# Kernel tuning notes

Measured on AMD Instinct MI355X. Metric: run time of the kernel, lower is better.

The kernel has to match this reference:

```python
import jax, jax.numpy as jnp
import numpy as np

BATCH, INPUTDIM, OUTDIM, GRIDSIZE = 4096, 256, 256, 64


def setup_inputs() -> dict:
    key = jax.random.key(0)
    k1, k2 = jax.random.split(key)
    x = jax.random.normal(k1, (BATCH, INPUTDIM), dtype=jnp.float32)
    # xavier_uniform over (2, outdim, inputdim, gridsize): fan_in = inputdim*gridsize, fan_out = outdim*gridsize
    fan_in = INPUTDIM * GRIDSIZE
    fan_out = OUTDIM * GRIDSIZE
    limit = float(np.sqrt(6.0 / (fan_in + fan_out)))
    fouriercoeffs = jax.random.uniform(
        k2, (2, OUTDIM, INPUTDIM, GRIDSIZE), dtype=jnp.float32,
        minval=-limit, maxval=limit)
    bias = jnp.zeros((1, OUTDIM), dtype=jnp.float32)
    return {"x": x, "fouriercoeffs": fouriercoeffs, "bias": bias}


def reference(x, fouriercoeffs, bias):
    # x: [B, inputdim]; fouriercoeffs: [2, outdim, inputdim, gridsize]; bias: [1, outdim]
    # gridsize_param is clamp/round'ed to an int in torch -> static = initial_gridsize here.
    G = fouriercoeffs.shape[-1]
    k = jnp.arange(1, G + 1, dtype=x.dtype)        # [G] frequencies 1..G
    xk = x[:, :, None] * k                          # [B, inputdim, G]
    c = jnp.cos(xk)                                 # [B, inputdim, G]
    s = jnp.sin(xk)                                 # [B, inputdim, G]
    # Fused contraction over (inputdim, gridsize) -- avoids the naive
    # [B, outdim, inputdim, gridsize] broadcast tensor of the torch code.
    y = (jnp.einsum('big,oig->bo', c, fouriercoeffs[0])
         + jnp.einsum('big,oig->bo', s, fouriercoeffs[1])
         + bias)                                    # [B, outdim]
    return y
```

## Files before the change

### kernel.cpp

```cpp
#include <hip/hip_runtime.h>
#include <hip/hip_bf16.h>


typedef __attribute__((ext_vector_type(8))) short short8;
typedef __attribute__((ext_vector_type(16))) float f32x16;

#define SPLITK 16
#define ICHUNK (256 / SPLITK)

#define INV2PI 0.15915494309189535f

__device__ __forceinline__ unsigned short f2bf(float f) {
    unsigned u = __builtin_bit_cast(unsigned, f);
    u += 0x7fffu + ((u >> 16) & 1u);
    return (unsigned short)(u >> 16);
}
#if __has_builtin(__builtin_amdgcn_cvt_pk_bf16_f32)
typedef __attribute__((ext_vector_type(2))) __bf16 bf16x2_t;
__device__ __forceinline__ unsigned pkbf16(float a, float b) {
    bf16x2_t v = __builtin_amdgcn_cvt_pk_bf16_f32(a, b);
    return __builtin_bit_cast(unsigned, v);
}
#else
__device__ __forceinline__ unsigned pkbf16(float a, float b) {
    unsigned ua = __builtin_bit_cast(unsigned, a) + 0x8000u;
    unsigned ub = __builtin_bit_cast(unsigned, b) + 0x8000u;
    return __builtin_amdgcn_perm(ub, ua, 0x07060302u);
}
#endif

__device__ __forceinline__ void dbl2(float c, float s, float& co, float& so) {
    float t = c + c;
    co = __builtin_fmaf(t, c, -1.f);
    so = t * s;
}
__device__ __forceinline__ void rot2(float c, float s, float cr, float sr,
                                     float& co, float& so) {
    float t = s * sr;
    co = __builtin_fmaf(c, cr, -t);
    float u = s * cr;
    so = __builtin_fmaf(c, sr, u);
}

__device__ __forceinline__ short8 chain8(float m1, float fm1, float f0) {
    unsigned r[4];
    float vp = fm1, v = f0;
    #pragma unroll
    for (int h = 0; h < 4; ++h) {
        float v1 = __builtin_fmaf(m1, v, -vp);
        r[h] = pkbf16(v, v1);
        float v2 = __builtin_fmaf(m1, v1, -v);
        vp = v1; v = v2;
    }
    uint4 u; u.x = r[0]; u.y = r[1]; u.z = r[2]; u.w = r[3];
    return __builtin_bit_cast(short8, u);
}

__device__ __forceinline__ void async_load16(const void* g, void* l) {
    __builtin_amdgcn_global_load_lds(
        (const __attribute__((address_space(1))) unsigned int*)g,
        (__attribute__((address_space(3))) unsigned int*)l,
        16, 0, 0);
}

__global__ __launch_bounds__(512) void prep_kernel(
    const float* __restrict__ fc, unsigned short* __restrict__ ws2)
{
    __shared__ unsigned pk[512][36];
    const int i = blockIdx.x;
    const int t = threadIdx.x;
    const int rr  = t >> 4;
    const int l16 = t & 15;

    #pragma unroll
    for (int p = 0; p < 16; ++p) {
        int r = p * 32 + rr;
        const float4* src =
            (const float4*)(fc + ((size_t)r * 256 + i) * 64) + l16;
        float4 v = *src;
        pk[r][l16 * 2]     = pkbf16(v.x, v.y);
        pk[r][l16 * 2 + 1] = pkbf16(v.z, v.w);
    }
    __syncthreads();

    #pragma unroll
    for (int gg = 0; gg < 8; ++gg) {
        int gi = gg * 512 + t;
        int sog = gi >> 6, ll = gi & 63;
        int ks = sog >> 3, cb = sog & 7;
        int o  = cb * 32 + (ll & 31);
        int kb = ks * 16 + (ll >> 5) * 8;
        int tt = kb >> 6, g0 = kb & 63;
        int r = tt * 256 + o;
        int c = g0 >> 1;
        uint4 v;
        v.x = pk[r][c]; v.y = pk[r][c + 1];
        v.z = pk[r][c + 2]; v.w = pk[r][c + 3];
        ((uint4*)ws2)[(size_t)i * 4096 + gi] = v;
    }
}

__global__ __launch_bounds__(256) void bias_init(
    const float* __restrict__ bias, float* __restrict__ out)
{
    int idx4 = blockIdx.x * 256 + threadIdx.x;
    ((float4*)out)[idx4] = ((const float4*)bias)[idx4 & 63];
}

__global__ __launch_bounds__(256) void reduce_kernel(
    const unsigned short* __restrict__ pws, const float* __restrict__ bias,
    float* __restrict__ out)
{
    int idx4 = blockIdx.x * 256 + threadIdx.x;
    float4 r = ((const float4*)bias)[idx4 & 63];
    #pragma unroll
    for (int z = 0; z < SPLITK; ++z) {
        ushort4 v = ((const ushort4*)pws)[(size_t)z * 262144 + idx4];
        r.x += __builtin_bit_cast(float, (unsigned)v.x << 16);
        r.y += __builtin_bit_cast(float, (unsigned)v.y << 16);
        r.z += __builtin_bit_cast(float, (unsigned)v.z << 16);
        r.w += __builtin_bit_cast(float, (unsigned)v.w << 16);
    }
    ((float4*)out)[idx4] = r;
}

template <bool USE_WS, bool PARTIAL>
__global__ __launch_bounds__(512, 2) void fkan_gemm(
    const float* __restrict__ x, const float* __restrict__ fc,
    const unsigned short* __restrict__ bws, float* __restrict__ out,
    unsigned short* __restrict__ pws)
{
    __shared__ uint4 Bflat[8192];
    __shared__ float xs[ICHUNK][256];

    const int t  = threadIdx.x;
    const int l  = t & 63;
    const int w  = t >> 6;
    const int rg = w >> 1;
    const int cg = w & 1;
    const int m32 = l & 31;
    const int h  = l >> 5;

    const int bid = blockIdx.x;
    const int z   = bid & 15;
    const int bx  = bid >> 4;
    const int rowBase = bx * 256;
    const int iBase   = z * ICHUNK;

    f32x16 acc[2][4];
    #pragma unroll
    for (int a = 0; a < 2; ++a)
        #pragma unroll
        for (int b = 0; b < 4; ++b) acc[a][b] = (f32x16)0.0f;

    short8 aF[2][8];

    auto stageHalf = [&](int slot, int j) {
        const uint4* base = (const uint4*)bws +
            (size_t)(iBase + (j >> 1)) * 4096 + (j & 1) * 2048;
        uint4* dst = Bflat + slot * 2048;
        #pragma unroll
        for (int cc = 0; cc < 4; ++cc) {
            int c = cc * 8 + w;
            async_load16(base + (size_t)c * 64 + l, (void*)(dst + c * 64));
        }
    };

    auto synth = [&](int ii) {
        #pragma unroll
        for (int rf = 0; rf < 2; ++rf) {
            float xv = xs[ii][rg * 64 + rf * 32 + m32];
            float rev = xv * INV2PI;
            float s1 = __builtin_amdgcn_sinf(rev);
            float c1 = __builtin_amdgcn_cosf(rev);
            const float m1 = c1 + c1;
            float c2, s2, c4, s4, c8, s8, c16, s16;
            dbl2(c1, s1, c2, s2);
            dbl2(c2, s2, c4, s4);
            dbl2(c4, s4, c8, s8);
            dbl2(c8, s8, c16, s16);
            float cB = h ? c8 : 1.f;
            float sB = h ? s8 : 0.f;
            #pragma unroll
            for (int k = 0; k < 4; ++k) {
                float cB1, sB1;
                rot2(cB, sB, c1, s1, cB1, sB1);
                aF[rf][k]     = chain8(m1, cB, cB1);
                aF[rf][4 + k] = chain8(m1, sB, sB1);
                if (k < 3) {
                    float cN, sN;
                    rot2(cB, sB, c16, s16, cN, sN);
                    cB = cN; sB = sN;
                }
            }
        }
    };

    auto mfmaHalf = [&](int slot,
                        short8 a00, short8 a01, short8 a02, short8 a03,
                        short8 a10, short8 a11, short8 a12, short8 a13) {
        const uint4* Bp = Bflat + slot * 2048;
        short8 a0v[4] = {a00, a01, a02, a03};
        short8 a1v[4] = {a10, a11, a12, a13};
        #pragma unroll
        for (int ks = 0; ks < 4; ++ks) {
            short8 bF[4];
            #pragma unroll
            for (int cf = 0; cf < 4; ++cf)
                bF[cf] = __builtin_bit_cast(short8,
                    Bp[(ks * 8 + cg * 4 + cf) * 64 + l]);
            #pragma unroll
            for (int cf = 0; cf < 4; ++cf) {
                acc[0][cf] = __builtin_amdgcn_mfma_f32_32x32x16_bf16(
                    a0v[ks], bF[cf], acc[0][cf], 0, 0, 0);
                acc[1][cf] = __builtin_amdgcn_mfma_f32_32x32x16_bf16(
                    a1v[ks], bF[cf], acc[1][cf], 0, 0, 0);
            }
        }
    };

    auto loadXs = [&]() {
        const int row = t >> 1;
        const int hf  = t & 1;
        const float4* px =
            (const float4*)(x + (size_t)(rowBase + row) * 256 + iBase) + hf * 2;
        float4 v0 = px[0], v1 = px[1];
        int c0 = hf * 8;
        xs[c0 + 0][row] = v0.x; xs[c0 + 1][row] = v0.y;
        xs[c0 + 2][row] = v0.z; xs[c0 + 3][row] = v0.w;
        xs[c0 + 4][row] = v1.x; xs[c0 + 5][row] = v1.y;
        xs[c0 + 6][row] = v1.z; xs[c0 + 7][row] = v1.w;
    };

    if constexpr (USE_WS) {
        loadXs();
        stageHalf(0, 0);
        stageHalf(1, 1);
        stageHalf(2, 2);
        asm volatile("s_waitcnt vmcnt(8) lgkmcnt(0)" ::: "memory");
        __builtin_amdgcn_s_barrier();
        asm volatile("" ::: "memory");

        #pragma unroll 1
        for (int jj = 0; jj < 16; ++jj) {
            const int j0 = jj * 2;

            if (jj <= 14) stageHalf((j0 + 3) & 3, j0 + 3);
            synth(jj);
            __builtin_amdgcn_s_setprio(1);
            mfmaHalf(j0 & 3,
                     aF[0][0], aF[0][1], aF[0][2], aF[0][3],
                     aF[1][0], aF[1][1], aF[1][2], aF[1][3]);
            __builtin_amdgcn_s_setprio(0);
            if (jj < 15) asm volatile("s_waitcnt vmcnt(8)" ::: "memory");
            else         asm volatile("s_waitcnt vmcnt(0)" ::: "memory");
            __builtin_amdgcn_s_barrier();
            asm volatile("" ::: "memory");

            if (jj <= 13) stageHalf((j0 + 4) & 3, j0 + 4);
            __builtin_amdgcn_s_setprio(1);
            mfmaHalf((j0 + 1) & 3,
                     aF[0][4], aF[0][5], aF[0][6], aF[0][7],
                     aF[1][4], aF[1][5], aF[1][6], aF[1][7]);
            __builtin_amdgcn_s_setprio(0);
            if (jj < 14) {
                asm volatile("s_waitcnt vmcnt(8)" ::: "memory");
                __builtin_amdgcn_s_barrier();
                asm volatile("" ::: "memory");
            } else if (jj == 14) {
                asm volatile("s_waitcnt vmcnt(4)" ::: "memory");
                __builtin_amdgcn_s_barrier();
                asm volatile("" ::: "memory");
            }
        }
    } else {
        auto stageBfc = [&](int p, int i) {
            #pragma unroll
            for (int gg = 0; gg < 8; ++gg) {
                int gi  = gg * 512 + t;
                int sog = gi >> 6, ll = gi & 63;
                int ks = sog >> 3, cb = sog & 7;
                int o  = cb * 32 + (ll & 31);
                int kb = ks * 16 + (ll >> 5) * 8;
                int tt = kb >> 6, g0 = kb & 63;
                const float4* p4 = (const float4*)(fc +
                    ((((size_t)tt * 256 + o) * 256 + i) * 64 + g0));
                float4 a = p4[0], b = p4[1];
                uint4 v;
                v.x = pkbf16(a.x, a.y); v.y = pkbf16(a.z, a.w);
                v.z = pkbf16(b.x, b.y); v.w = pkbf16(b.z, b.w);
                Bflat[p * 4096 + gi] = v;
            }
        };
        stageBfc(0, iBase);
        loadXs();
        __syncthreads();
        #pragma unroll 1
        for (int ii = 0; ii < ICHUNK; ++ii) {
            const int p = ii & 1;
            if (ii + 1 < ICHUNK) stageBfc(p ^ 1, iBase + ii + 1);
            synth(ii);
            mfmaHalf(p * 2,
                     aF[0][0], aF[0][1], aF[0][2], aF[0][3],
                     aF[1][0], aF[1][1], aF[1][2], aF[1][3]);
            mfmaHalf(p * 2 + 1,
                     aF[0][4], aF[0][5], aF[0][6], aF[0][7],
                     aF[1][4], aF[1][5], aF[1][6], aF[1][7]);
            __syncthreads();
        }
    }

    const int r0 = rowBase + rg * 64 + h * 4;
    const int c0 = cg * 128 + m32;
    if (PARTIAL) {
        unsigned short* dst = pws + (size_t)z * (4096u * 256u);
        #pragma unroll
        for (int rf = 0; rf < 2; ++rf)
            #pragma unroll
            for (int cf = 0; cf < 4; ++cf)
                #pragma unroll
                for (int e = 0; e < 16; ++e) {
                    int rl = (e & 3) + 8 * (e >> 2);
                    dst[(size_t)(r0 + rf * 32 + rl) * 256 + (c0 + cf * 32)] =
                        f2bf(acc[rf][cf][e]);
                }
    } else {
        #pragma unroll
        for (int rf = 0; rf < 2; ++rf)
            #pragma unroll
            for (int cf = 0; cf < 4; ++cf)
                #pragma unroll
                for (int e = 0; e < 16; ++e) {
                    int rl = (e & 3) + 8 * (e >> 2);
                    atomicAdd(out + (size_t)(r0 + rf * 32 + rl) * 256 + (c0 + cf * 32),
                              acc[rf][cf][e]);
                }
    }
}

extern "C" void kernel_launch(void* const* d_in, const int* in_sizes, int n_in,
                              void* d_out, int out_size, void* d_ws, size_t ws_size,
                              hipStream_t stream) {
    const float* x    = (const float*)d_in[0];
    const float* fc   = (const float*)d_in[1];
    const float* bias = (const float*)d_in[2];
    float* out = (float*)d_out;
    unsigned short* bws = (unsigned short*)d_ws;

    const size_t wsCoeff = (size_t)256 * 4096 * 16;
    const size_t wsFull  = wsCoeff + (size_t)SPLITK * 4096 * 256 * 2;
    unsigned short* pws = (unsigned short*)((char*)d_ws + wsCoeff);

    if (ws_size >= wsFull) {
        hipLaunchKernelGGL(prep_kernel, dim3(256), dim3(512), 0, stream, fc, bws);
        hipLaunchKernelGGL((fkan_gemm<true, true>), dim3(256), dim3(512), 0, stream,
                           x, fc, bws, out, pws);
        hipLaunchKernelGGL(reduce_kernel, dim3(1024), dim3(256), 0, stream,
                           pws, bias, out);
    } else if (ws_size >= wsCoeff) {
        hipLaunchKernelGGL(bias_init, dim3(1024), dim3(256), 0, stream, bias, out);
        hipLaunchKernelGGL(prep_kernel, dim3(256), dim3(512), 0, stream, fc, bws);
        hipLaunchKernelGGL((fkan_gemm<true, false>), dim3(256), dim3(512), 0, stream,
                           x, fc, bws, out, pws);
    } else {
        hipLaunchKernelGGL(bias_init, dim3(1024), dim3(256), 0, stream, bias, out);
        hipLaunchKernelGGL((fkan_gemm<false, false>), dim3(256), dim3(512), 0, stream,
                           x, fc, bws, out, pws);
    }
}
```

Baseline: 156.9 us.

## Split Fourier synthesis into cos ladder and sin chains, software-pipeline across MFMA halves

The per-iteration sin/cos synthesis is split in two. The cosine ladder for the next input column is computed during the sine-half MFMAs, and the sine chains are computed just before the cosine-half MFMAs, so the VALU work interleaves with the matrix ops instead of running as one block ahead of them. It also drops the s_setprio raises around the MFMA sections. In exchange it keeps extra rotation state per lane (cB/sB per k, c1/s1/m1), which raises register pressure.

```diff
diff --git a/kernel.cpp b/kernel.cpp
--- a/kernel.cpp
+++ b/kernel.cpp
@@ -153,7 +153,10 @@
         #pragma unroll
         for (int b = 0; b < 4; ++b) acc[a][b] = (f32x16)0.0f;
 
-    short8 aF[2][8];
+    short8 aFc[2][4];
+    short8 aFs[2][4];
+    float m1v[2], c1v[2], s1v[2];
+    float cBv[2][4], sBv[2][4];
 
     auto stageHalf = [&](int slot, int j) {
         const uint4* base = (const uint4*)bws +
@@ -166,7 +169,7 @@
         }
     };
 
-    auto synth = [&](int ii) {
+    auto ladderCos = [&](int ii) {
         #pragma unroll
         for (int rf = 0; rf < 2; ++rf) {
             float xv = xs[ii][rg * 64 + rf * 32 + m32];
@@ -181,17 +184,30 @@
             dbl2(c8, s8, c16, s16);
             float cB = h ? c8 : 1.f;
             float sB = h ? s8 : 0.f;
+            m1v[rf] = m1; c1v[rf] = c1; s1v[rf] = s1;
             #pragma unroll
             for (int k = 0; k < 4; ++k) {
+                cBv[rf][k] = cB; sBv[rf][k] = sB;
                 float cB1, sB1;
                 rot2(cB, sB, c1, s1, cB1, sB1);
-                aF[rf][k]     = chain8(m1, cB, cB1);
-                aF[rf][4 + k] = chain8(m1, sB, sB1);
+                aFc[rf][k] = chain8(m1, cB, cB1);
                 if (k < 3) {
                     float cN, sN;
                     rot2(cB, sB, c16, s16, cN, sN);
                     cB = cN; sB = sN;
                 }
+            }
+        }
+    };
+
+    auto sinChains = [&]() {
+        #pragma unroll
+        for (int rf = 0; rf < 2; ++rf) {
+            #pragma unroll
+            for (int k = 0; k < 4; ++k) {
+                float cB = cBv[rf][k], sB = sBv[rf][k];
+                float sB1 = __builtin_fmaf(cB, s1v[rf], sB * c1v[rf]);
+                aFs[rf][k] = chain8(m1v[rf], sB, sB1);
             }
         }
     };
@@ -241,28 +257,27 @@
         __builtin_amdgcn_s_barrier();
         asm volatile("" ::: "memory");
 
+        ladderCos(0);
+
         #pragma unroll 1
         for (int jj = 0; jj < 16; ++jj) {
             const int j0 = jj * 2;
 
             if (jj <= 14) stageHalf((j0 + 3) & 3, j0 + 3);
-            synth(jj);
-            __builtin_amdgcn_s_setprio(1);
+            sinChains();
             mfmaHalf(j0 & 3,
-                     aF[0][0], aF[0][1], aF[0][2], aF[0][3],
-                     aF[1][0], aF[1][1], aF[1][2], aF[1][3]);
-            __builtin_amdgcn_s_setprio(0);
+                     aFc[0][0], aFc[0][1], aFc[0][2], aFc[0][3],
+                     aFc[1][0], aFc[1][1], aFc[1][2], aFc[1][3]);
             if (jj < 15) asm volatile("s_waitcnt vmcnt(8)" ::: "memory");
             else         asm volatile("s_waitcnt vmcnt(0)" ::: "memory");
             __builtin_amdgcn_s_barrier();
             asm volatile("" ::: "memory");
 
             if (jj <= 13) stageHalf((j0 + 4) & 3, j0 + 4);
-            __builtin_amdgcn_s_setprio(1);
+            ladderCos((jj + 1) & 15);
             mfmaHalf((j0 + 1) & 3,
-                     aF[0][4], aF[0][5], aF[0][6], aF[0][7],
-                     aF[1][4], aF[1][5], aF[1][6], aF[1][7]);
-            __builtin_amdgcn_s_setprio(0);
+                     aFs[0][0], aFs[0][1], aFs[0][2], aFs[0][3],
+                     aFs[1][0], aFs[1][1], aFs[1][2], aFs[1][3]);
             if (jj < 14) {
                 asm volatile("s_waitcnt vmcnt(8)" ::: "memory");
                 __builtin_amdgcn_s_barrier();
@@ -299,13 +314,14 @@
         for (int ii = 0; ii < ICHUNK; ++ii) {
             const int p = ii & 1;
             if (ii + 1 < ICHUNK) stageBfc(p ^ 1, iBase + ii + 1);
-            synth(ii);
+            ladderCos(ii);
+            sinChains();
             mfmaHalf(p * 2,
-                     aF[0][0], aF[0][1], aF[0][2], aF[0][3],
-                     aF[1][0], aF[1][1], aF[1][2], aF[1][3]);
+                     aFc[0][0], aFc[0][1], aFc[0][2], aFc[0][3],
+                     aFc[1][0], aFc[1][1], aFc[1][2], aFc[1][3]);
             mfmaHalf(p * 2 + 1,
-                     aF[0][4], aF[0][5], aF[0][6], aF[0][7],
-                     aF[1][4], aF[1][5], aF[1][6], aF[1][7]);
+                     aFs[0][0], aFs[0][1], aFs[0][2], aFs[0][3],
+                     aFs[1][0], aFs[1][1], aFs[1][2], aFs[1][3]);
             __syncthreads();
         }
     }
```

Result: no change. 156.4 us (-0.4%).
